# Performance work log

Hardware: AMD Instinct MI355X
Metric: run time of the kernel (lower is better)

Reference implementation:

```python
import math
import jax, jax.numpy as jnp
import numpy as np

B, A, M, NC = 32, 8400, 32, 80
TOP_K, ALPHA, BETA, EPS = 13, 1.0, 6.0, 1e-9
IMG = 640.0


def _ciou(b1, b2, eps=1e-7):
    # b1, b2 broadcastable [..., 4]; CIoU as in compute_iou (box1=gt, box2=pred)
    b1x1, b1y1, b1x2, b1y2 = b1[..., 0], b1[..., 1], b1[..., 2], b1[..., 3]
    b2x1, b2y1, b2x2, b2y2 = b2[..., 0], b2[..., 1], b2[..., 2], b2[..., 3]
    w1, h1 = b1x2 - b1x1, b1y2 - b1y1 + eps
    w2, h2 = b2x2 - b2x1, b2y2 - b2y1 + eps
    inter = (jnp.minimum(b1x2, b2x2) - jnp.maximum(b1x1, b2x1)).clip(0) * \
            (jnp.minimum(b1y2, b2y2) - jnp.maximum(b1y1, b2y1)).clip(0)
    union = w1 * h1 + w2 * h2 - inter + eps
    iou = inter / union
    cw = jnp.maximum(b1x2, b2x2) - jnp.minimum(b1x1, b2x1)
    ch = jnp.maximum(b1y2, b2y2) - jnp.minimum(b1y1, b2y1)
    c2 = cw ** 2 + ch ** 2 + eps
    rho2 = ((b2x1 + b2x2 - b1x1 - b1x2) ** 2 + (b2y1 + b2y2 - b1y1 - b1y2) ** 2) / 4.0
    v = (4.0 / math.pi ** 2) * (jnp.arctan(w2 / h2) - jnp.arctan(w1 / h1)) ** 2
    alpha = jax.lax.stop_gradient(v / (v - iou + (1.0 + eps)))
    return iou - (rho2 / c2 + v * alpha)


def setup_inputs() -> dict:
    key = jax.random.key(0)
    ks = jax.random.split(key, 8)
    pd_scores = jax.random.uniform(ks[0], (B, A, NC), jnp.float32)
    anc_points = jax.random.uniform(ks[1], (A, 2), jnp.float32) * IMG
    # predicted boxes around anchor points (valid x1<x2, y1<y2)
    off = jax.random.uniform(ks[2], (B, A, 4), jnp.float32) * 80.0 + 2.0
    pd_bboxes = jnp.concatenate([anc_points[None] - off[..., :2],
                                 anc_points[None] + off[..., 2:]], -1)
    # GT boxes: random centers and sizes, clipped to image
    c = jax.random.uniform(ks[3], (B, M, 2), jnp.float32) * IMG
    wh = jax.random.uniform(ks[4], (B, M, 2), jnp.float32) * 180.0 + 20.0
    gt_bboxes = jnp.concatenate([(c - wh / 2).clip(0, IMG), (c + wh / 2).clip(0, IMG)], -1)
    gt_labels = jax.random.randint(ks[5], (B, M, 1), 0, NC, jnp.int64)
    n_valid = jax.random.randint(ks[6], (B,), 1, M + 1)
    mask_gt = (jnp.arange(M)[None, :] < n_valid[:, None]).astype(jnp.float32)[..., None]
    return {"pd_scores": pd_scores, "pd_bboxes": pd_bboxes, "anc_points": anc_points,
            "gt_labels": gt_labels, "gt_bboxes": gt_bboxes, "mask_gt": mask_gt}


def reference(pd_scores, pd_bboxes, anc_points, gt_labels, gt_bboxes, mask_gt):
    b, a, nc = pd_scores.shape
    m = gt_bboxes.shape[1]
    dtype = pd_scores.dtype

    # anchors-inside-GT mask: [B,M,A]
    lt = gt_bboxes[:, :, None, :2]          # [B,M,1,2]
    rb = gt_bboxes[:, :, None, 2:]
    deltas = jnp.concatenate([anc_points[None, None] - lt,
                              rb - anc_points[None, None]], -1)  # [B,M,A,4]
    mask_in_gts = deltas.min(-1) > EPS
    mg = mask_gt[..., 0] > 0                 # [B,M] bool
    gt_mask = mask_in_gts & mg[:, :, None]

    # per-GT class score gather: pd_scores[b, :, gt_labels[b,m]] -> [B,M,A]
    labels = gt_labels[..., 0]               # [B,M]
    idx = jnp.broadcast_to(labels[:, :, None, None], (b, m, a, 1))
    gathered = jnp.take_along_axis(jnp.broadcast_to(pd_scores[:, None], (b, m, a, nc)), idx, axis=3)[..., 0]
    bbox_scores = jnp.where(gt_mask, gathered, 0.0)

    # CIoU overlaps (dense, masked) [B,M,A]
    iou = _ciou(gt_bboxes[:, :, None, :], pd_bboxes[:, None, :, :])
    overlaps = jnp.where(gt_mask, jnp.maximum(iou, 0.0), 0.0)

    align_metric = bbox_scores ** ALPHA * overlaps ** BETA

    # top-k selection with duplicate suppression (faithful to scatter_add loop)
    _, tk_idx = jax.lax.top_k(align_metric, TOP_K)      # [B,M,K]
    tk_mask = jnp.broadcast_to(mg[:, :, None], tk_idx.shape)
    tk_idx = jnp.where(tk_mask, tk_idx, 0)
    bi = jnp.arange(b)[:, None, None]
    mi = jnp.arange(m)[None, :, None]
    counts = jnp.zeros((b, m, a), jnp.int32).at[bi, mi, tk_idx].add(1)
    mask_top_k = jnp.where(counts > 1, 0, counts).astype(dtype)

    mask_pos = mask_top_k * mask_in_gts.astype(dtype) * mg[:, :, None].astype(dtype)
    fg_mask = mask_pos.sum(1)                            # [B,A]

    # resolve anchors assigned to multiple GTs (no-op when none; matches torch branch)
    mask_multi = fg_mask[:, None, :] > 1                 # [B,M,A] (broadcast)
    max_idx = overlaps.argmax(1)                         # [B,A]
    is_max = (jnp.arange(m)[None, :, None] == max_idx[:, None, :]).astype(dtype)
    mask_pos = jnp.where(mask_multi, is_max, mask_pos)
    fg_mask = mask_pos.sum(1)

    target_gt_idx = mask_pos.argmax(1)                   # [B,A]
    target_labels = jnp.maximum(jnp.take_along_axis(labels, target_gt_idx, axis=1), 0)
    target_bboxes = jnp.take_along_axis(
        gt_bboxes, jnp.broadcast_to(target_gt_idx[..., None], (b, a, 4)), axis=1)

    target_scores = jax.nn.one_hot(target_labels, NC, dtype=dtype)
    target_scores = jnp.where((fg_mask > 0)[..., None], target_scores, 0.0)

    am = align_metric * mask_pos
    pos_am = am.max(-1, keepdims=True)                   # [B,M,1]
    pos_ov = (overlaps * mask_pos).max(-1, keepdims=True)
    norm = (am * pos_ov / (pos_am + EPS)).max(1)[..., None]  # [B,A,1]
    target_scores = target_scores * norm

    return target_bboxes, target_scores, fg_mask > 0
```

## Files before the change

### kernel.cpp

```cpp
#include <hip/hip_runtime.h>
#include <math.h>

#define BB 32
#define AA 8400
#define MM 32
#define NCC 80
#define TOPK 13
#define CAP 1024
#define NW (AA / 32 + 1)

__device__ __forceinline__ void wave_argmax(float& v, int& i) {
    #pragma unroll
    for (int off = 32; off > 0; off >>= 1) {
        float ov = __shfl_xor(v, off, 64);
        int oi = __shfl_xor(i, off, 64);
        if (ov > v || (ov == v && oi < i)) { v = ov; i = oi; }
    }
}

__global__ __launch_bounds__(256) void k0_zero(unsigned int* __restrict__ selmask) {
    int g = blockIdx.x * 256 + threadIdx.x;
    if (g < BB * AA / 4) reinterpret_cast<uint4*>(selmask)[g] = uint4{0u, 0u, 0u, 0u};
}

__global__ __launch_bounds__(256) void k12_topk(
        const float* __restrict__ pd_scores, const float* __restrict__ pd_bboxes,
        const float* __restrict__ anc, const int* __restrict__ gt_labels,
        const float* __restrict__ gt_bboxes, const float* __restrict__ mask_gt,
        unsigned int* __restrict__ selmask, float* __restrict__ pos_am, float* __restrict__ pos_ov) {
    __shared__ float lval[CAP];
    __shared__ int   lidx[CAP];
    __shared__ unsigned int bmask[NW];
    __shared__ float wv[4];
    __shared__ int   wi[4];
    __shared__ int   wsum[4];
    __shared__ int   s_p;
    const float eps = 1e-7f;
    int bm = blockIdx.x;
    int b = bm >> 5;
    int m = bm & 31;
    unsigned int mbit = 1u << m;
    int tid = threadIdx.x;
    int lane = tid & 63;
    int wid = tid >> 6;
    if (tid == 0) pos_am[bm] = 0.f;
    if (tid == 1) pos_ov[bm] = 0.f;
    if (!(mask_gt[bm] > 0.f)) return;
    if (tid == 2) s_p = 0;

    for (int i = tid; i < NW; i += 256) bmask[i] = 0u;
    float4 g = reinterpret_cast<const float4*>(gt_bboxes)[bm];

    const float4* anc4 = reinterpret_cast<const float4*>(anc);
    unsigned long long bits = 0ull;
    int c_t = 0;
    #pragma unroll
    for (int j = 0; j < 17; j++) {
        int e = tid + (j << 8);
        if (e < 4200) {
            float4 an = anc4[e];
            float d0 = fminf(fminf(an.x - g.x, an.y - g.y), fminf(g.z - an.x, g.w - an.y));
            float d1 = fminf(fminf(an.z - g.x, an.w - g.y), fminf(g.z - an.z, g.w - an.w));
            if (d0 > 1e-9f) { bits |= 1ull << (2 * j);     c_t++; }
            if (d1 > 1e-9f) { bits |= 1ull << (2 * j + 1); c_t++; }
        }
    }
    int x = c_t;
    #pragma unroll
    for (int off = 1; off < 64; off <<= 1) {
        int y = __shfl_up(x, off, 64);
        if (lane >= off) x += y;
    }
    if (lane == 63) wsum[wid] = x;
    __syncthreads();
    int base = 0;
    #pragma unroll
    for (int w = 0; w < 4; w++) if (w < wid) base += wsum[w];
    int n_c = min(wsum[0] + wsum[1] + wsum[2] + wsum[3], CAP);
    {
        int o = base + x - c_t;
        unsigned long long mm_ = bits;
        while (mm_) {
            int k = __builtin_ctzll(mm_);
            mm_ &= mm_ - 1ull;
            int i = 2 * tid + 512 * (k >> 1) + (k & 1);
            if (o < CAP) lidx[o] = i;
            o++;
        }
    }
    for (int s = n_c + tid; s < CAP; s += 256) { lval[s] = -1.f; lidx[s] = AA; }
    __syncthreads();

    float w1 = g.z - g.x, h1 = g.w - g.y + eps;
    float atg = atanf(w1 / h1);
    float w1h1 = w1 * h1;
    float sgx = g.x + g.z, sgy = g.y + g.w;
    int lab = gt_labels[bm];
    const float4* pbb = reinterpret_cast<const float4*>(pd_bboxes) + (long)b * AA;
    const float* scp = pd_scores + (long)b * AA * NCC + lab;
    int nit = (n_c + 255) >> 8;
    for (int it = 0; it < nit; it++) {
        int s = (it << 8) + tid;
        bool pos = false;
        if (s < n_c) {
            int i = lidx[s];
            float4 pb = pbb[i];
            float w2 = pb.z - pb.x, h2 = pb.w - pb.y + eps;
            float iw = fmaxf(fminf(g.z, pb.z) - fmaxf(g.x, pb.x), 0.f);
            float ih = fmaxf(fminf(g.w, pb.w) - fmaxf(g.y, pb.y), 0.f);
            float inter = iw * ih;
            float uni = w1h1 + w2 * h2 - inter + eps;
            float iou = inter / uni;
            float cw = fmaxf(g.z, pb.z) - fminf(g.x, pb.x);
            float ch = fmaxf(g.w, pb.w) - fminf(g.y, pb.y);
            float c2 = cw * cw + ch * ch + eps;
            float dx = pb.x + pb.z - sgx, dy = pb.y + pb.w - sgy;
            float rho2 = (dx * dx + dy * dy) * 0.25f;
            float dv = atanf(w2 / h2) - atg;
            float v = 0.4052847345693511f * dv * dv;
            float alpha = v / (v - iou + (1.0f + eps));
            float cv = iou - (rho2 / c2 + v * alpha);
            float ov = fmaxf(cv, 0.f);
            float sc = scp[(long)i * NCC];
            float o2 = ov * ov;
            float val = sc * o2 * o2 * o2;
            pos = val > 0.f;
            lval[s] = pos ? val : -1.f;
            if (pos) atomicOr(&bmask[i >> 5], 1u << (i & 31));
        }
        unsigned long long pm = __ballot(pos);
        if (lane == 0) atomicAdd(&s_p, (int)__popcll(pm));
    }
    __syncthreads();
    int p = s_p;

    if (p >= TOPK) {
        float v0 = lval[tid], v1 = lval[tid + 256], v2 = lval[tid + 512], v3 = lval[tid + 768];
        int   i0 = lidx[tid], i1 = lidx[tid + 256], i2 = lidx[tid + 512], i3 = lidx[tid + 768];
        for (int k = 0; k < TOPK; k++) {
            float bv = v0; int bi = i0;
            if (v1 > bv || (v1 == bv && i1 < bi)) { bv = v1; bi = i1; }
            if (v2 > bv || (v2 == bv && i2 < bi)) { bv = v2; bi = i2; }
            if (v3 > bv || (v3 == bv && i3 < bi)) { bv = v3; bi = i3; }
            wave_argmax(bv, bi);
            if (lane == 0) { wv[wid] = bv; wi[wid] = bi; }
            __syncthreads();
            float gv = wv[0]; int gi = wi[0];
            #pragma unroll
            for (int w = 1; w < 4; w++) {
                float ov = wv[w]; int oi = wi[w];
                if (ov > gv || (ov == gv && oi < gi)) { gv = ov; gi = oi; }
            }
            if (tid == 0) atomicOr(&selmask[b * AA + gi], mbit);
            if (i0 == gi) v0 = -1.f;
            if (i1 == gi) v1 = -1.f;
            if (i2 == gi) v2 = -1.f;
            if (i3 == gi) v3 = -1.f;
            __syncthreads();
        }
    } else {
        for (int s = tid; s < n_c; s += 256)
            if (lval[s] > 0.f) atomicOr(&selmask[b * AA + lidx[s]], mbit);
        if (wid == 0) {
            int need = TOPK - p;
            for (int base_i = 0; need > 0 && base_i < AA; base_i += 64) {
                int i = base_i + lane;
                bool cand = (i < AA) && !((bmask[i >> 5] >> (i & 31)) & 1u);
                unsigned long long wm = __ballot(cand);
                int take = min(need, (int)__popcll(wm));
                if (cand && (int)__popcll(wm & ((1ull << lane) - 1ull)) < take) {
                    float2 an = reinterpret_cast<const float2*>(anc)[i];
                    float dmin = fminf(fminf(an.x - g.x, an.y - g.y), fminf(g.z - an.x, g.w - an.y));
                    if (dmin > 1e-9f) atomicOr(&selmask[b * AA + i], mbit);
                }
                need -= take;
            }
        }
    }
}

__global__ __launch_bounds__(256) void k3_resolve(
        const float* __restrict__ pd_scores, const float* __restrict__ pd_bboxes,
        const float* __restrict__ anc, const int* __restrict__ gt_labels,
        const float* __restrict__ gt_bboxes, const float* __restrict__ mask_gt,
        const unsigned int* __restrict__ selmask,
        float* __restrict__ pos_am, float* __restrict__ pos_ov,
        float* __restrict__ out_bbox, float* __restrict__ out_fg,
        float* __restrict__ amval, int* __restrict__ packed) {
    __shared__ float sg[MM][8];
    __shared__ int slab[MM];
    __shared__ int smg[MM];
    const float eps = 1e-7f;
    int b = blockIdx.y;
    int tid = threadIdx.x;
    if (tid < MM) {
        int gm = b * MM + tid;
        float4 g = reinterpret_cast<const float4*>(gt_bboxes)[gm];
        float w1 = g.z - g.x, h1 = g.w - g.y + eps;
        sg[tid][0] = g.x; sg[tid][1] = g.y; sg[tid][2] = g.z; sg[tid][3] = g.w;
        sg[tid][4] = w1 * h1;
        sg[tid][5] = atanf(w1 / h1);
        sg[tid][6] = g.x + g.z;
        sg[tid][7] = g.y + g.w;
        int lb = gt_labels[gm]; if (lb < 0) lb = 0;
        slab[tid] = lb;
        smg[tid] = mask_gt[gm] > 0.f ? 1 : 0;
    }
    __syncthreads();
    int a = blockIdx.x * 256 + tid;
    if (a >= AA) return;
    int g = b * AA + a;
    unsigned int sel = selmask[g];
    int fg = __popc(sel);

    int tg = 0; bool fgo = false; float ovt = 0.f;
    if (fg >= 1) {
        float ax = anc[a * 2], ay = anc[a * 2 + 1];
        float4 pb = reinterpret_cast<const float4*>(pd_bboxes)[g];
        float w2 = pb.z - pb.x, h2 = pb.w - pb.y + eps;
        float atp = atanf(w2 / h2);
        float w2h2 = w2 * h2;
        float spx = pb.x + pb.z, spy = pb.y + pb.w;
        fgo = true;
        if (fg == 1) {
            tg = __ffs(sel) - 1;
            float gx1 = sg[tg][0], gy1 = sg[tg][1], gx2 = sg[tg][2], gy2 = sg[tg][3];
            float iw = fmaxf(fminf(gx2, pb.z) - fmaxf(gx1, pb.x), 0.f);
            float ih = fmaxf(fminf(gy2, pb.w) - fmaxf(gy1, pb.y), 0.f);
            float inter = iw * ih;
            float uni = sg[tg][4] + w2h2 - inter + eps;
            float iou = inter / uni;
            float cw = fmaxf(gx2, pb.z) - fminf(gx1, pb.x);
            float ch = fmaxf(gy2, pb.w) - fminf(gy1, pb.y);
            float c2 = cw * cw + ch * ch + eps;
            float dx = spx - sg[tg][6], dy = spy - sg[tg][7];
            float rho2 = (dx * dx + dy * dy) * 0.25f;
            float dv = atp - sg[tg][5];
            float v = 0.4052847345693511f * dv * dv;
            float alpha = v / (v - iou + (1.0f + eps));
            ovt = fmaxf(iou - (rho2 / c2 + v * alpha), 0.f);
        } else {
            float bestov = -1.f; int bestm = 0;
            for (int mm = 0; mm < MM; mm++) {
                float gx1 = sg[mm][0], gy1 = sg[mm][1], gx2 = sg[mm][2], gy2 = sg[mm][3];
                float dmin = fminf(fminf(ax - gx1, ay - gy1), fminf(gx2 - ax, gy2 - ay));
                float ov = 0.f;
                if ((dmin > 1e-9f) && smg[mm]) {
                    float iw = fmaxf(fminf(gx2, pb.z) - fmaxf(gx1, pb.x), 0.f);
                    float ih = fmaxf(fminf(gy2, pb.w) - fmaxf(gy1, pb.y), 0.f);
                    float inter = iw * ih;
                    float uni = sg[mm][4] + w2h2 - inter + eps;
                    float iou = inter / uni;
                    float cw = fmaxf(gx2, pb.z) - fminf(gx1, pb.x);
                    float ch = fmaxf(gy2, pb.w) - fminf(gy1, pb.y);
                    float c2 = cw * cw + ch * ch + eps;
                    float dx = spx - sg[mm][6], dy = spy - sg[mm][7];
                    float rho2 = (dx * dx + dy * dy) * 0.25f;
                    float dv = atp - sg[mm][5];
                    float v = 0.4052847345693511f * dv * dv;
                    float alpha = v / (v - iou + (1.0f + eps));
                    ov = fmaxf(iou - (rho2 / c2 + v * alpha), 0.f);
                }
                if (ov > bestov) { bestov = ov; bestm = mm; }
            }
            tg = bestm; ovt = bestov;
        }
    }

    float4 gb; gb.x = sg[tg][0]; gb.y = sg[tg][1]; gb.z = sg[tg][2]; gb.w = sg[tg][3];
    reinterpret_cast<float4*>(out_bbox)[g] = gb;
    out_fg[g] = fgo ? 1.f : 0.f;
    float amv = 0.f;
    if (fgo) {
        float sc = pd_scores[(long)g * NCC + slab[tg]];
        float o2 = ovt * ovt;
        amv = sc * o2 * o2 * o2;
        atomicMax((int*)&pos_am[b * MM + tg], __float_as_int(amv));
        atomicMax((int*)&pos_ov[b * MM + tg], __float_as_int(ovt));
    }
    amval[g] = amv;
    packed[g] = tg | (slab[tg] << 8) | ((fgo ? 1 : 0) << 16);
}

__global__ __launch_bounds__(256) void k4_scores(
        const float* __restrict__ amval, const int* __restrict__ packed,
        const float* __restrict__ pos_am, const float* __restrict__ pos_ov,
        float* __restrict__ out_scores) {
    int g = blockIdx.x * 256 + threadIdx.x;
    const int NQ = NCC / 4;
    if (g >= BB * AA * NQ) return;
    int ba = g / NQ;
    int c0 = (g % NQ) * 4;
    float4 o = {0.f, 0.f, 0.f, 0.f};
    int p = packed[ba];
    if (p & (1 << 16)) {
        int tg = p & 31, lab = (p >> 8) & 127;
        int b = ba / AA;
        int bm = b * MM + tg;
        float nv = (amval[ba] * pos_ov[bm]) / (pos_am[bm] + 1e-9f);
        int d = lab - c0;
        if (d == 0) o.x = nv; else if (d == 1) o.y = nv;
        else if (d == 2) o.z = nv; else if (d == 3) o.w = nv;
    }
    reinterpret_cast<float4*>(out_scores)[g] = o;
}

extern "C" void kernel_launch(void* const* d_in, const int* in_sizes, int n_in,
                              void* d_out, int out_size, void* d_ws, size_t ws_size,
                              hipStream_t stream) {
    const float* pd_scores = (const float*)d_in[0];
    const float* pd_bboxes = (const float*)d_in[1];
    const float* anc       = (const float*)d_in[2];
    const int*   gt_labels = (const int*)d_in[3];
    const float* gt_bboxes = (const float*)d_in[4];
    const float* mask_gt   = (const float*)d_in[5];

    const long nBA = (long)BB * AA;

    char* ws = (char*)d_ws;
    unsigned int* selmask = (unsigned int*)ws;  ws += nBA * 4;
    float* pos_am = (float*)ws;                 ws += BB * MM * 4;
    float* pos_ov = (float*)ws;                 ws += BB * MM * 4;
    float* amval  = (float*)ws;                 ws += nBA * 4;
    int*   packed = (int*)ws;                   ws += nBA * 4;

    float* out_bbox   = (float*)d_out;
    float* out_scores = out_bbox + nBA * 4;
    float* out_fg     = out_scores + nBA * NCC;

    k0_zero<<<(int)((nBA / 4 + 255) / 256), 256, 0, stream>>>(selmask);
    k12_topk<<<BB * MM, 256, 0, stream>>>(pd_scores, pd_bboxes, anc, gt_labels,
                                          gt_bboxes, mask_gt, selmask, pos_am, pos_ov);
    dim3 g3((AA + 255) / 256, BB);
    k3_resolve<<<g3, 256, 0, stream>>>(pd_scores, pd_bboxes, anc, gt_labels,
                                       gt_bboxes, mask_gt, selmask, pos_am, pos_ov,
                                       out_bbox, out_fg, amval, packed);
    long nS4 = nBA * (NCC / 4);
    k4_scores<<<(int)((nS4 + 255) / 256), 256, 0, stream>>>(amval, packed, pos_am, pos_ov, out_scores);
}
```

Measured before the change: 190.5 us.

## Replace dense selection bitmask with sparse per-GT index lists and pack metadata

The top-k kernel now writes up to 16 selected anchor indices per GT instead of OR-ing bits into a dense B×A mask. This removes the zeroing kernel and the global atomics. The resolve kernel rebuilds each block's 256-anchor selection columns in shared memory by scanning that batch's 512 indices. amval and packed are merged into one int2 buffer, and the large output stores use nontemporal hints. The cost is an extra scan of the index list in every resolve block.

```diff
diff --git a/kernel.cpp b/kernel.cpp
--- a/kernel.cpp
+++ b/kernel.cpp
@@ -9,6 +9,8 @@
 #define CAP 1024
 #define NW (AA / 32 + 1)
 
+typedef float nfloat4 __attribute__((ext_vector_type(4)));
+
 __device__ __forceinline__ void wave_argmax(float& v, int& i) {
     #pragma unroll
     for (int off = 32; off > 0; off >>= 1) {
@@ -18,35 +20,30 @@
     }
 }
 
-__global__ __launch_bounds__(256) void k0_zero(unsigned int* __restrict__ selmask) {
-    int g = blockIdx.x * 256 + threadIdx.x;
-    if (g < BB * AA / 4) reinterpret_cast<uint4*>(selmask)[g] = uint4{0u, 0u, 0u, 0u};
-}
-
 __global__ __launch_bounds__(256) void k12_topk(
         const float* __restrict__ pd_scores, const float* __restrict__ pd_bboxes,
         const float* __restrict__ anc, const int* __restrict__ gt_labels,
         const float* __restrict__ gt_bboxes, const float* __restrict__ mask_gt,
-        unsigned int* __restrict__ selmask, float* __restrict__ pos_am, float* __restrict__ pos_ov) {
+        int* __restrict__ sel_idx, float* __restrict__ pos_am, float* __restrict__ pos_ov) {
     __shared__ float lval[CAP];
     __shared__ int   lidx[CAP];
     __shared__ unsigned int bmask[NW];
     __shared__ float wv[4];
     __shared__ int   wi[4];
     __shared__ int   wsum[4];
-    __shared__ int   s_p;
+    __shared__ int   s_p, s_sel;
     const float eps = 1e-7f;
     int bm = blockIdx.x;
     int b = bm >> 5;
-    int m = bm & 31;
-    unsigned int mbit = 1u << m;
     int tid = threadIdx.x;
     int lane = tid & 63;
     int wid = tid >> 6;
     if (tid == 0) pos_am[bm] = 0.f;
     if (tid == 1) pos_ov[bm] = 0.f;
+    if (tid == 2) s_p = 0;
+    if (tid == 3) s_sel = 0;
+    if (tid < 16) sel_idx[bm * 16 + tid] = -1;
     if (!(mask_gt[bm] > 0.f)) return;
-    if (tid == 2) s_p = 0;
 
     for (int i = tid; i < NW; i += 256) bmask[i] = 0u;
     float4 g = reinterpret_cast<const float4*>(gt_bboxes)[bm];
@@ -105,6 +102,7 @@
         if (s < n_c) {
             int i = lidx[s];
             float4 pb = pbb[i];
+            float sc = scp[(long)i * NCC];
             float w2 = pb.z - pb.x, h2 = pb.w - pb.y + eps;
             float iw = fmaxf(fminf(g.z, pb.z) - fmaxf(g.x, pb.x), 0.f);
             float ih = fmaxf(fminf(g.w, pb.w) - fmaxf(g.y, pb.y), 0.f);
@@ -121,7 +119,6 @@
             float alpha = v / (v - iou + (1.0f + eps));
             float cv = iou - (rho2 / c2 + v * alpha);
             float ov = fmaxf(cv, 0.f);
-            float sc = scp[(long)i * NCC];
             float o2 = ov * ov;
             float val = sc * o2 * o2 * o2;
             pos = val > 0.f;
@@ -137,6 +134,7 @@
     if (p >= TOPK) {
         float v0 = lval[tid], v1 = lval[tid + 256], v2 = lval[tid + 512], v3 = lval[tid + 768];
         int   i0 = lidx[tid], i1 = lidx[tid + 256], i2 = lidx[tid + 512], i3 = lidx[tid + 768];
+        int mysel = -1;
         for (int k = 0; k < TOPK; k++) {
             float bv = v0; int bi = i0;
             if (v1 > bv || (v1 == bv && i1 < bi)) { bv = v1; bi = i1; }
@@ -151,16 +149,20 @@
                 float ov = wv[w]; int oi = wi[w];
                 if (ov > gv || (ov == gv && oi < gi)) { gv = ov; gi = oi; }
             }
-            if (tid == 0) atomicOr(&selmask[b * AA + gi], mbit);
+            if (tid == k) mysel = gi;
             if (i0 == gi) v0 = -1.f;
             if (i1 == gi) v1 = -1.f;
             if (i2 == gi) v2 = -1.f;
             if (i3 == gi) v3 = -1.f;
             __syncthreads();
         }
+        if (tid < TOPK) sel_idx[bm * 16 + tid] = mysel;
     } else {
         for (int s = tid; s < n_c; s += 256)
-            if (lval[s] > 0.f) atomicOr(&selmask[b * AA + lidx[s]], mbit);
+            if (lval[s] > 0.f) {
+                int slot = atomicAdd(&s_sel, 1);
+                sel_idx[bm * 16 + slot] = lidx[s];
+            }
         if (wid == 0) {
             int need = TOPK - p;
             for (int base_i = 0; need > 0 && base_i < AA; base_i += 64) {
@@ -171,7 +173,10 @@
                 if (cand && (int)__popcll(wm & ((1ull << lane) - 1ull)) < take) {
                     float2 an = reinterpret_cast<const float2*>(anc)[i];
                     float dmin = fminf(fminf(an.x - g.x, an.y - g.y), fminf(g.z - an.x, g.w - an.y));
-                    if (dmin > 1e-9f) atomicOr(&selmask[b * AA + i], mbit);
+                    if (dmin > 1e-9f) {
+                        int slot = atomicAdd(&s_sel, 1);
+                        sel_idx[bm * 16 + slot] = i;
+                    }
                 }
                 need -= take;
             }
@@ -183,13 +188,14 @@
         const float* __restrict__ pd_scores, const float* __restrict__ pd_bboxes,
         const float* __restrict__ anc, const int* __restrict__ gt_labels,
         const float* __restrict__ gt_bboxes, const float* __restrict__ mask_gt,
-        const unsigned int* __restrict__ selmask,
+        const int* __restrict__ sel_idx,
         float* __restrict__ pos_am, float* __restrict__ pos_ov,
         float* __restrict__ out_bbox, float* __restrict__ out_fg,
-        float* __restrict__ amval, int* __restrict__ packed) {
+        int2* __restrict__ meta) {
     __shared__ float sg[MM][8];
     __shared__ int slab[MM];
     __shared__ int smg[MM];
+    __shared__ unsigned int selcol[256];
     const float eps = 1e-7f;
     int b = blockIdx.y;
     int tid = threadIdx.x;
@@ -206,11 +212,20 @@
         slab[tid] = lb;
         smg[tid] = mask_gt[gm] > 0.f ? 1 : 0;
     }
-    __syncthreads();
-    int a = blockIdx.x * 256 + tid;
+    selcol[tid] = 0u;
+    __syncthreads();
+    int a0 = blockIdx.x * 256;
+    const int* sl = sel_idx + b * MM * 16;
+    #pragma unroll
+    for (int t = tid; t < MM * 16; t += 256) {
+        int e = sl[t];
+        if (e >= a0 && e < a0 + 256) atomicOr(&selcol[e - a0], 1u << (t >> 4));
+    }
+    __syncthreads();
+    int a = a0 + tid;
     if (a >= AA) return;
     int g = b * AA + a;
-    unsigned int sel = selmask[g];
+    unsigned int sel = selcol[tid];
     int fg = __popc(sel);
 
     int tg = 0; bool fgo = false; float ovt = 0.f;
@@ -267,8 +282,8 @@
         }
     }
 
-    float4 gb; gb.x = sg[tg][0]; gb.y = sg[tg][1]; gb.z = sg[tg][2]; gb.w = sg[tg][3];
-    reinterpret_cast<float4*>(out_bbox)[g] = gb;
+    nfloat4 gb = {sg[tg][0], sg[tg][1], sg[tg][2], sg[tg][3]};
+    __builtin_nontemporal_store(gb, reinterpret_cast<nfloat4*>(out_bbox) + g);
     out_fg[g] = fgo ? 1.f : 0.f;
     float amv = 0.f;
     if (fgo) {
@@ -278,12 +293,11 @@
         atomicMax((int*)&pos_am[b * MM + tg], __float_as_int(amv));
         atomicMax((int*)&pos_ov[b * MM + tg], __float_as_int(ovt));
     }
-    amval[g] = amv;
-    packed[g] = tg | (slab[tg] << 8) | ((fgo ? 1 : 0) << 16);
+    meta[g] = make_int2(__float_as_int(amv), tg | (slab[tg] << 8) | ((fgo ? 1 : 0) << 16));
 }
 
 __global__ __launch_bounds__(256) void k4_scores(
-        const float* __restrict__ amval, const int* __restrict__ packed,
+        const int2* __restrict__ meta,
         const float* __restrict__ pos_am, const float* __restrict__ pos_ov,
         float* __restrict__ out_scores) {
     int g = blockIdx.x * 256 + threadIdx.x;
@@ -291,18 +305,19 @@
     if (g >= BB * AA * NQ) return;
     int ba = g / NQ;
     int c0 = (g % NQ) * 4;
-    float4 o = {0.f, 0.f, 0.f, 0.f};
-    int p = packed[ba];
+    nfloat4 o = {0.f, 0.f, 0.f, 0.f};
+    int2 mt = meta[ba];
+    int p = mt.y;
     if (p & (1 << 16)) {
         int tg = p & 31, lab = (p >> 8) & 127;
         int b = ba / AA;
         int bm = b * MM + tg;
-        float nv = (amval[ba] * pos_ov[bm]) / (pos_am[bm] + 1e-9f);
+        float nv = (__int_as_float(mt.x) * pos_ov[bm]) / (pos_am[bm] + 1e-9f);
         int d = lab - c0;
         if (d == 0) o.x = nv; else if (d == 1) o.y = nv;
         else if (d == 2) o.z = nv; else if (d == 3) o.w = nv;
     }
-    reinterpret_cast<float4*>(out_scores)[g] = o;
+    __builtin_nontemporal_store(o, reinterpret_cast<nfloat4*>(out_scores) + g);
 }
 
 extern "C" void kernel_launch(void* const* d_in, const int* in_sizes, int n_in,
@@ -318,23 +333,21 @@
     const long nBA = (long)BB * AA;
 
     char* ws = (char*)d_ws;
-    unsigned int* selmask = (unsigned int*)ws;  ws += nBA * 4;
-    float* pos_am = (float*)ws;                 ws += BB * MM * 4;
-    float* pos_ov = (float*)ws;                 ws += BB * MM * 4;
-    float* amval  = (float*)ws;                 ws += nBA * 4;
-    int*   packed = (int*)ws;                   ws += nBA * 4;
+    int*   sel_idx = (int*)ws;                  ws += (long)BB * MM * 16 * 4;
+    float* pos_am  = (float*)ws;                ws += BB * MM * 4;
+    float* pos_ov  = (float*)ws;                ws += BB * MM * 4;
+    int2*  meta    = (int2*)ws;                 ws += nBA * 8;
 
     float* out_bbox   = (float*)d_out;
     float* out_scores = out_bbox + nBA * 4;
     float* out_fg     = out_scores + nBA * NCC;
 
-    k0_zero<<<(int)((nBA / 4 + 255) / 256), 256, 0, stream>>>(selmask);
     k12_topk<<<BB * MM, 256, 0, stream>>>(pd_scores, pd_bboxes, anc, gt_labels,
-                                          gt_bboxes, mask_gt, selmask, pos_am, pos_ov);
+                                          gt_bboxes, mask_gt, sel_idx, pos_am, pos_ov);
     dim3 g3((AA + 255) / 256, BB);
     k3_resolve<<<g3, 256, 0, stream>>>(pd_scores, pd_bboxes, anc, gt_labels,
-                                       gt_bboxes, mask_gt, selmask, pos_am, pos_ov,
-                                       out_bbox, out_fg, amval, packed);
+                                       gt_bboxes, mask_gt, sel_idx, pos_am, pos_ov,
+                                       out_bbox, out_fg, meta);
     long nS4 = nBA * (NCC / 4);
-    k4_scores<<<(int)((nS4 + 255) / 256), 256, 0, stream>>>(amval, packed, pos_am, pos_ov, out_scores);
-}
+    k4_scores<<<(int)((nS4 + 255) / 256), 256, 0, stream>>>(meta, pos_am, pos_ov, out_scores);
+}
```

New measurement: 187.6 us. No clear change (-1.5%).
